# Performance work log

Measured on AMD Instinct MI355X. Metric: run time of the kernel, lower is better.

## Reference

```python
import jax, jax.numpy as jnp
import numpy as np

B, C4, H, W = 2, 128, 128, 128
POOL_SIZE = 10


def setup_inputs() -> dict:
    key = jax.random.key(0)
    k1, k2, k3 = jax.random.split(key, 3)
    feature = jax.random.normal(k1, (B, C4, H, W), dtype=jnp.float32)
    K = H * W
    # valid boxes: x1<x2, y1<y2, inside the feature map
    xy1 = jax.random.uniform(k2, (B, K, 2), dtype=jnp.float32) * jnp.array([W * 0.5, H * 0.5], jnp.float32)
    wh = jax.random.uniform(k3, (B, K, 2), dtype=jnp.float32) * jnp.array([W * 0.45, H * 0.45], jnp.float32) + 1.0
    boxes = jnp.concatenate([xy1, xy1 + wh], axis=-1)  # [B, K, 4] = (x1,y1,x2,y2)
    return {"feature": feature, "boxes": boxes, "pool_size": POOL_SIZE}


def reference(feature, boxes, pool_size):
    # feature: [B, 4*C, H, W]; boxes: [B, K, 4]; output: [B, C, K, 4]
    Bn, C4n, Hn, Wn = feature.shape
    C = C4n // 4
    K = boxes.shape[1]
    P = pool_size + 1
    x1, y1, x2, y2 = (boxes[..., i] for i in range(4))  # each [B, K]
    t = jnp.arange(P, dtype=feature.dtype) / pool_size  # [P]
    sx = x1[..., None] + t * (x2 - x1)[..., None]  # [B, K, P] along-x samples
    sy = y1[..., None] + t * (y2 - y1)[..., None]  # [B, K, P] along-y samples
    cx1 = jnp.broadcast_to(x1[..., None], sx.shape)
    cx2 = jnp.broadcast_to(x2[..., None], sx.shape)
    cy1 = jnp.broadcast_to(y1[..., None], sy.shape)
    cy2 = jnp.broadcast_to(y2[..., None], sy.shape)
    # border order: 0=top (y=y1), 1=left (x=x1), 2=bottom (y=y2), 3=right (x=x2)
    xs = jnp.stack([sx, cx1, sx, cx2], axis=1)  # [B, 4, K, P]
    ys = jnp.stack([cy1, sy, cy2, sy], axis=1)  # [B, 4, K, P]

    valid = (xs > -1.0) & (xs < Wn) & (ys > -1.0) & (ys < Hn)
    x = jnp.clip(xs, 0.0, Wn - 1)
    y = jnp.clip(ys, 0.0, Hn - 1)
    x0 = jnp.floor(x).astype(jnp.int32)
    y0 = jnp.floor(y).astype(jnp.int32)
    x1i = jnp.minimum(x0 + 1, Wn - 1)
    y1i = jnp.minimum(y0 + 1, Hn - 1)
    lx = (x - x0)[:, :, None]  # [B, 4, 1, K, P]
    ly = (y - y0)[:, :, None]

    featf = feature.reshape(Bn, 4, C, Hn * Wn)  # channel group g feeds border g

    def gather(yi, xi):
        idx = (yi * Wn + xi).reshape(Bn, 4, 1, K * P)
        return jnp.take_along_axis(featf, idx, axis=3).reshape(Bn, 4, C, K, P)

    val = (gather(y0, x0) * (1 - ly) * (1 - lx)
           + gather(y0, x1i) * (1 - ly) * lx
           + gather(y1i, x0) * ly * (1 - lx)
           + gather(y1i, x1i) * ly * lx)
    val = jnp.where(valid[:, :, None], val, 0.0)
    out = val.max(axis=-1)  # max-pool over the P samples per border -> [B, 4, C, K]
    return out.transpose(0, 2, 3, 1)  # [B, C, K, 4]
```

## Files before the change

kernel.cpp:

```cpp
#include <hip/hip_runtime.h>
#include <math.h>

#define BN   2
#define CG   32
#define HH   128
#define WW   128
#define HWSZ (HH*WW)
#define KK   16384
#define CHUNK 256
#define NCHK 2
#define SORTB 64
#define SEGCAP 32

#define WS_F16_OFF   (0u)
#define WS_TMP_OFF   (8u << 20)
#define WS_BKT_OFF   (16u << 20)
#define WS_CNT_OFF   (32u << 20)
#define WS_NEED      ((32u << 20) + (128u << 10))

typedef float vf4 __attribute__((ext_vector_type(4)));
typedef _Float16 h8 __attribute__((ext_vector_type(8)));

__device__ inline unsigned int pack_h2(float a, float b) {
  unsigned short ua = __builtin_bit_cast(unsigned short, (_Float16)a);
  unsigned short ub = __builtin_bit_cast(unsigned short, (_Float16)b);
  return (unsigned int)ua | ((unsigned int)ub << 16);
}

__global__ __launch_bounds__(256) void sort_transpose_kernel(
    const float* __restrict__ feat, unsigned short* __restrict__ ws,
    const float* __restrict__ boxes, unsigned int* __restrict__ cnt,
    uint4* __restrict__ bkt) {
  __shared__ uint2 smem[128 * 9];
  const int blk = blockIdx.x;
  const int t   = threadIdx.x;

  if (blk < SORTB) {
    unsigned int* hist = (unsigned int*)smem;
    const int batch = blk >> 5;
    const int seg   = blk & 31;
    const int k0    = seg * 512;
    hist[t] = 0u; hist[t + 256] = 0u;
    __syncthreads();

    vf4 bx[2];
    unsigned short rnk[2][4];
    int bin[2][4];
#pragma unroll
    for (int i = 0; i < 2; ++i) {
      const int k = k0 + i * 256 + t;
      bx[i] = *(const vf4*)(boxes + ((size_t)batch * KK + k) * 4);
#pragma unroll
      for (int g = 0; g < 4; ++g) {
        const float fix = (g == 0) ? bx[i][1] : (g == 1) ? bx[i][0]
                         : (g == 2) ? bx[i][3] : bx[i][2];
        const int f0 = (int)fminf(fmaxf(fix, 0.0f), 127.0f);
        bin[i][g] = (g << 7) | f0;
        rnk[i][g] = (unsigned short)atomicAdd(&hist[bin[i][g]], 1u);
      }
    }
    __syncthreads();

    cnt[(size_t)((batch << 9) + t) * 32 + seg]       = min(hist[t], (unsigned)SEGCAP);
    cnt[(size_t)((batch << 9) + t + 256) * 32 + seg] = min(hist[t + 256], (unsigned)SEGCAP);

#pragma unroll
    for (int i = 0; i < 2; ++i) {
      const int k = k0 + i * 256 + t;
#pragma unroll
      for (int g = 0; g < 4; ++g) {
        if (rnk[i][g] < SEGCAP) {
          const bool horiz = (g & 1) == 0;
          const float fix = (g == 0) ? bx[i][1] : (g == 1) ? bx[i][0]
                           : (g == 2) ? bx[i][3] : bx[i][2];
          const float fc = fminf(fmaxf(fix, 0.0f), 127.0f);
          const int f0 = bin[i][g] & 127;
          const float mov_s = horiz ? bx[i][0] : bx[i][1];
          const float mov_d = horiz ? (bx[i][2] - bx[i][0]) : (bx[i][3] - bx[i][1]);
          const float lf    = fc - (float)f0;
          const bool  fok   = (fix > -1.0f) && (fix < 128.0f);
          uint4 rec;
          rec.x = __builtin_bit_cast(unsigned int, mov_s);
          rec.y = __builtin_bit_cast(unsigned int, mov_d);
          rec.z = __builtin_bit_cast(unsigned int, lf);
          rec.w = (unsigned int)k | (fok ? 0x80000000u : 0u);
          const int gbin = (batch << 9) + bin[i][g];
          bkt[(size_t)gbin * (32 * SEGCAP) + seg * SEGCAP + rnk[i][g]] = rec;
        }
      }
    }
  } else {
    uint2* lds = smem;
    const int idx = blk - SORTB;
    const int s  = idx & 7;
    const int i0 = (idx >> 3) * 128;

    const int iL = (t & 31) * 4;
    const int cq = t >> 5;

    const float* src = feat + (size_t)s * (CG * HWSZ) + i0 + iL;
    vf4 r[4];
#pragma unroll
    for (int cc = 0; cc < 4; ++cc)
      r[cc] = *(const vf4*)(src + (size_t)(cq * 4 + cc) * HWSZ);

#pragma unroll
    for (int ii = 0; ii < 4; ++ii) {
      uint2 q;
      q.x = pack_h2(r[0][ii], r[1][ii]);
      q.y = pack_h2(r[2][ii], r[3][ii]);
      lds[(iL + ii) * 9 + cq] = q;
    }
    __syncthreads();

    uint2* dst = (uint2*)(ws + ((size_t)s * HWSZ + i0) * CG);
    const int q2 = t & 7;
    const int ih = t >> 3;
#pragma unroll
    for (int it = 0; it < 4; ++it) {
      const int i = ih + 32 * it;
      dst[i * 8 + q2] = lds[i * 9 + q2];
    }
  }
}

__global__ __launch_bounds__(256) void border_gather_binned(
    const unsigned short* __restrict__ wsu,
    const unsigned int* __restrict__ cnt, const uint4* __restrict__ bkt,
    const int* __restrict__ psp, unsigned short* __restrict__ tmp) {
  __shared__ _Float16 tile[2 * 128 * 40];
  __shared__ uint4 recs[CHUNK];
  __shared__ unsigned int segbase[33];
  __shared__ float stf[64];

  const int blk  = blockIdx.x;
  const int s    = blk & 7;
  const int f0   = (blk >> 3) & 127;
  const int ch   = blk >> 10;
  const int g    = s & 3;
  const int b    = s >> 2;
  const int gbin = s * 128 + f0;
  const int t    = threadIdx.x;

  if (t < 64) {
    unsigned int c = 0u;
    if (t < 32) c = min(cnt[(size_t)gbin * 32 + t], (unsigned)SEGCAP);
    unsigned int x = c;
#pragma unroll
    for (int d = 1; d < 32; d <<= 1) {
      unsigned int y = __shfl_up(x, d, 64);
      if (t >= d) x += y;
    }
    if (t < 32) {
      segbase[t] = x - c;
      if (t == 31) segbase[32] = x;
    }
  }
  __syncthreads();

  const int n  = (int)segbase[32];
  const int i0 = ch * CHUNK;
  const int i1 = min(n, i0 + CHUNK);
  if (i1 <= i0) return;

  const int ps = *psp;
  if (t < 64) stf[t] = (float)(t <= ps ? t : ps) / (float)ps;

  const bool horiz = (g & 1) == 0;
  const int f1 = min(f0 + 1, 127);
  const _Float16* slab = (const _Float16*)wsu + (size_t)s * (HWSZ * CG);

#pragma unroll
  for (int it = 0; it < 4; ++it) {
    const int chunk = it * 256 + t;
    const int cc   = chunk >> 9;
    const int rem  = chunk & 511;
    const int p    = rem >> 2;
    const int slot = rem & 3;
    const int fcc  = cc ? f1 : f0;
    const size_t srci = horiz ? ((size_t)(fcc * 128 + p) * 32)
                              : ((size_t)(p * 128 + fcc) * 32);
    const uint4 v = *(const uint4*)(slab + srci + slot * 8);
    *(uint4*)((char*)tile + cc * 10240 + p * 80 + slot * 16) = v;
  }

  {
    const int s2 = t >> 3;
    const int j  = t & 7;
    const int base = (int)segbase[s2];
    const int c    = (int)segbase[s2 + 1] - base;
    for (int l = j; l < c; l += 8) {
      const int pos = base + l;
      if (pos >= i0 && pos < i1)
        recs[pos - i0] = bkt[(size_t)gbin * (32 * SEGCAP) + s2 * SEGCAP + l];
    }
  }
  __syncthreads();

  const int w      = t >> 6;
  const int oct    = t & 3;
  const int slot16 = (t >> 2) & 15;

  for (int base = i0 + w * 16; base < i1; base += 64) {
    const int ii  = base + slot16;
    const bool vb = ii < i1;
    const uint4 rec = recs[vb ? (ii - i0) : 0];
    const float mov_s = __builtin_bit_cast(float, rec.x);
    const float mov_d = __builtin_bit_cast(float, rec.y);
    const float lf    = __builtin_bit_cast(float, rec.z);
    const bool  fok   = (rec.w >> 31) != 0u;
    const int   kid   = (int)(rec.w & 0xFFFFu);

    h8 acc = (h8)(_Float16)(-65504.0f);

#define SAMPLE(TP) do {                                                    \
      const float mov = fmaf((TP), mov_d, mov_s);                          \
      const bool ok = fok && (mov > -1.0f) && (mov < 128.0f);              \
      const float mc = fminf(fmaxf(mov, 0.0f), 127.0f);                    \
      const int m0 = (int)mc;                                              \
      const float lm = mc - (float)m0;                                     \
      const int m1 = min(m0 + 1, 127);                                     \
      const int a0 = m0 * 80 + oct * 16;                                   \
      const int a1 = m1 * 80 + oct * 16;                                   \
      const h8 f00 = *(const h8*)((const char*)tile + a0);                 \
      const h8 f01 = *(const h8*)((const char*)tile + a1);                 \
      const h8 f10 = *(const h8*)((const char*)tile + 10240 + a0);         \
      const h8 f11 = *(const h8*)((const char*)tile + 10240 + a1);         \
      const _Float16 w00 = (_Float16)((1.0f - lf) * (1.0f - lm));          \
      const _Float16 w01 = (_Float16)((1.0f - lf) * lm);                   \
      const _Float16 w10 = (_Float16)(lf * (1.0f - lm));                   \
      const _Float16 w11 = (_Float16)(lf * lm);                            \
      h8 v = f00 * w00 + f01 * w01 + f10 * w10 + f11 * w11;                \
      v = ok ? v : (h8)(_Float16)0.0f;                                     \
      acc = __builtin_elementwise_max(acc, v);                             \
    } while (0)

    if (ps == 10) {
#pragma unroll
      for (int p = 0; p <= 10; ++p) SAMPLE((float)p / 10.0f);
    } else {
      for (int p = 0; p <= ps; ++p) SAMPLE(stf[p]);
    }
#undef SAMPLE

    if (vb) {
      h8* dst = (h8*)(tmp + ((size_t)(b * 4 + g) * KK + kid) * 32 + oct * 8);
      *dst = acc;
    }
  }
}

__global__ __launch_bounds__(256) void untranspose_kernel(
    const unsigned short* __restrict__ tmp, float* __restrict__ out) {
  __shared__ float lds[4 * 32 * 33];
  const int blk = blockIdx.x;
  const int b   = blk >> 9;
  const int k0  = (blk & 511) * 32;
  const int t   = threadIdx.x;

#pragma unroll
  for (int it = 0; it < 2; ++it) {
    const int chunk = it * 256 + t;
    const int g   = chunk >> 7;
    const int rem = chunk & 127;
    const int kk  = rem >> 2;
    const int co8 = rem & 3;
    const h8 v = *(const h8*)((const _Float16*)tmp
                 + ((size_t)(b * 4 + g) * KK + k0 + kk) * 32 + co8 * 8);
#pragma unroll
    for (int j = 0; j < 8; ++j)
      lds[g * (32 * 33) + kk * 33 + co8 * 8 + j] = (float)v[j];
  }
  __syncthreads();

#pragma unroll
  for (int it = 0; it < 4; ++it) {
    const int chunk = it * 256 + t;
    const int c  = chunk >> 5;
    const int kk = chunk & 31;
    vf4 v;
#pragma unroll
    for (int g = 0; g < 4; ++g)
      v[g] = lds[g * (32 * 33) + kk * 33 + c];
    vf4* dst = (vf4*)(out + ((size_t)(b * CG + c) * KK + k0 + kk) * 4);
    __builtin_nontemporal_store(v, dst);
  }
}

__global__ __launch_bounds__(128) void border_align_fallback(
    const float* __restrict__ base, const float* __restrict__ boxes,
    const int* __restrict__ psp, float* __restrict__ out) {
  const int blk = blockIdx.x;
  const int b = blk >> 10;
  const int t = threadIdx.x;
  const int g = t >> 5, c = t & 31;
  const int k0 = (blk & 1023) * 16;
  const int ps = *psp;
  const float psf = (float)ps;
  const float* slab = base + (size_t)(b * 4 + g) * (CG * HWSZ) + (size_t)c * HWSZ;
  for (int kk = 0; kk < 16; ++kk) {
    const int kbox = k0 + kk;
    const float x1 = boxes[((size_t)b * KK + kbox) * 4 + 0];
    const float y1 = boxes[((size_t)b * KK + kbox) * 4 + 1];
    const float x2 = boxes[((size_t)b * KK + kbox) * 4 + 2];
    const float y2 = boxes[((size_t)b * KK + kbox) * 4 + 3];
    float m = -INFINITY;
    for (int p = 0; p <= ps; ++p) {
      const float tf = (float)p / psf;
      float x, y;
      if      (g == 0) { x = x1 + tf * (x2 - x1); y = y1; }
      else if (g == 1) { x = x1; y = y1 + tf * (y2 - y1); }
      else if (g == 2) { x = x1 + tf * (x2 - x1); y = y2; }
      else             { x = x2; y = y1 + tf * (y2 - y1); }
      const bool valid = (x > -1.0f) && (x < 128.0f) && (y > -1.0f) && (y < 128.0f);
      const float xc = fminf(fmaxf(x, 0.0f), 127.0f);
      const float yc = fminf(fmaxf(y, 0.0f), 127.0f);
      const int x0 = (int)xc, y0 = (int)yc;
      const float lx = xc - (float)x0, ly = yc - (float)y0;
      const int x1i = min(x0 + 1, 127), y1i = min(y0 + 1, 127);
      const float f00 = slab[y0 * WW + x0],  f01 = slab[y0 * WW + x1i];
      const float f10 = slab[y1i * WW + x0], f11 = slab[y1i * WW + x1i];
      float v = f00 * (1 - ly) * (1 - lx) + f01 * (1 - ly) * lx
              + f10 * ly * (1 - lx) + f11 * ly * lx;
      v = valid ? v : 0.0f;
      m = fmaxf(m, v);
    }
    out[(((size_t)(b * CG + c)) * KK + kbox) * 4 + g] = m;
  }
}

extern "C" void kernel_launch(void* const* d_in, const int* in_sizes, int n_in,
                              void* d_out, int out_size, void* d_ws, size_t ws_size,
                              hipStream_t stream) {
  const float* feature = (const float*)d_in[0];
  const float* boxes   = (const float*)d_in[1];
  const int*   psp     = (const int*)d_in[2];
  float*       out     = (float*)d_out;

  if (ws_size >= WS_NEED) {
    char* ws = (char*)d_ws;
    unsigned short* wsf16 = (unsigned short*)(ws + WS_F16_OFF);
    unsigned short* tmp   = (unsigned short*)(ws + WS_TMP_OFF);
    uint4*          bkt   = (uint4*)(ws + WS_BKT_OFF);
    unsigned int*   cnt   = (unsigned int*)(ws + WS_CNT_OFF);

    hipLaunchKernelGGL(sort_transpose_kernel, dim3(SORTB + 8 * (HWSZ / 128)),
                       dim3(256), 0, stream, feature, wsf16, boxes, cnt, bkt);
    hipLaunchKernelGGL(border_gather_binned, dim3(NCHK * 1024), dim3(256), 0,
                       stream, wsf16, cnt, bkt, psp, tmp);
    hipLaunchKernelGGL(untranspose_kernel, dim3(BN * 512), dim3(256), 0, stream,
                       tmp, out);
  } else {
    hipLaunchKernelGGL(border_align_fallback, dim3(BN * (KK / 16)), dim3(128), 0,
                       stream, feature, boxes, psp, out);
  }
}
```

Before: 91.52 us.

## Fuse three stages into one cooperative persistent kernel with grid syncs

New measurement: 336.3 us. 3.67x slower.

```diff
diff --git a/kernel.cpp b/kernel.cpp
--- a/kernel.cpp
+++ b/kernel.cpp
@@ -1,5 +1,8 @@
 #include <hip/hip_runtime.h>
+#include <hip/hip_cooperative_groups.h>
 #include <math.h>
+
+namespace cg = cooperative_groups;
 
 #define BN   2
 #define CG   32
@@ -11,6 +14,7 @@
 #define NCHK 2
 #define SORTB 64
 #define SEGCAP 32
+#define GRID 1024
 
 #define WS_F16_OFF   (0u)
 #define WS_TMP_OFF   (8u << 20)
@@ -18,6 +22,12 @@
 #define WS_CNT_OFF   (32u << 20)
 #define WS_NEED      ((32u << 20) + (128u << 10))
 
+#define SM_TILE   0
+#define SM_RECS   20480
+#define SM_SEGB   24576
+#define SM_STF    24712
+#define SM_SIZE   25088
+
 typedef float vf4 __attribute__((ext_vector_type(4)));
 typedef _Float16 h8 __attribute__((ext_vector_type(8)));
 
@@ -27,120 +37,115 @@
   return (unsigned int)ua | ((unsigned int)ub << 16);
 }
 
-__global__ __launch_bounds__(256) void sort_transpose_kernel(
-    const float* __restrict__ feat, unsigned short* __restrict__ ws,
-    const float* __restrict__ boxes, unsigned int* __restrict__ cnt,
-    uint4* __restrict__ bkt) {
-  __shared__ uint2 smem[128 * 9];
-  const int blk = blockIdx.x;
-  const int t   = threadIdx.x;
-
-  if (blk < SORTB) {
-    unsigned int* hist = (unsigned int*)smem;
-    const int batch = blk >> 5;
-    const int seg   = blk & 31;
-    const int k0    = seg * 512;
-    hist[t] = 0u; hist[t + 256] = 0u;
-    __syncthreads();
-
-    vf4 bx[2];
-    unsigned short rnk[2][4];
-    int bin[2][4];
-#pragma unroll
-    for (int i = 0; i < 2; ++i) {
-      const int k = k0 + i * 256 + t;
-      bx[i] = *(const vf4*)(boxes + ((size_t)batch * KK + k) * 4);
-#pragma unroll
-      for (int g = 0; g < 4; ++g) {
+
+__device__ __forceinline__ void sort_body(
+    char* smem, int v, const float* __restrict__ boxes,
+    unsigned int* __restrict__ cnt, uint4* __restrict__ bkt, int t) {
+  unsigned int* hist = (unsigned int*)smem;
+  const int batch = v >> 5;
+  const int seg   = v & 31;
+  const int k0    = seg * 512;
+  hist[t] = 0u; hist[t + 256] = 0u;
+  __syncthreads();
+
+  vf4 bx[2];
+  unsigned short rnk[2][4];
+  int bin[2][4];
+#pragma unroll
+  for (int i = 0; i < 2; ++i) {
+    const int k = k0 + i * 256 + t;
+    bx[i] = *(const vf4*)(boxes + ((size_t)batch * KK + k) * 4);
+#pragma unroll
+    for (int g = 0; g < 4; ++g) {
+      const float fix = (g == 0) ? bx[i][1] : (g == 1) ? bx[i][0]
+                       : (g == 2) ? bx[i][3] : bx[i][2];
+      const int f0 = (int)fminf(fmaxf(fix, 0.0f), 127.0f);
+      bin[i][g] = (g << 7) | f0;
+      rnk[i][g] = (unsigned short)atomicAdd(&hist[bin[i][g]], 1u);
+    }
+  }
+  __syncthreads();
+
+  cnt[(size_t)((batch << 9) + t) * 32 + seg]       = min(hist[t], (unsigned)SEGCAP);
+  cnt[(size_t)((batch << 9) + t + 256) * 32 + seg] = min(hist[t + 256], (unsigned)SEGCAP);
+
+#pragma unroll
+  for (int i = 0; i < 2; ++i) {
+    const int k = k0 + i * 256 + t;
+#pragma unroll
+    for (int g = 0; g < 4; ++g) {
+      if (rnk[i][g] < SEGCAP) {
+        const bool horiz = (g & 1) == 0;
         const float fix = (g == 0) ? bx[i][1] : (g == 1) ? bx[i][0]
                          : (g == 2) ? bx[i][3] : bx[i][2];
-        const int f0 = (int)fminf(fmaxf(fix, 0.0f), 127.0f);
-        bin[i][g] = (g << 7) | f0;
-        rnk[i][g] = (unsigned short)atomicAdd(&hist[bin[i][g]], 1u);
+        const float fc = fminf(fmaxf(fix, 0.0f), 127.0f);
+        const int f0 = bin[i][g] & 127;
+        const float mov_s = horiz ? bx[i][0] : bx[i][1];
+        const float mov_d = horiz ? (bx[i][2] - bx[i][0]) : (bx[i][3] - bx[i][1]);
+        const float lf    = fc - (float)f0;
+        const bool  fok   = (fix > -1.0f) && (fix < 128.0f);
+        uint4 rec;
+        rec.x = __builtin_bit_cast(unsigned int, mov_s);
+        rec.y = __builtin_bit_cast(unsigned int, mov_d);
+        rec.z = __builtin_bit_cast(unsigned int, lf);
+        rec.w = (unsigned int)k | (fok ? 0x80000000u : 0u);
+        const int gbin = (batch << 9) + bin[i][g];
+        bkt[(size_t)gbin * (32 * SEGCAP) + seg * SEGCAP + rnk[i][g]] = rec;
       }
     }
-    __syncthreads();
-
-    cnt[(size_t)((batch << 9) + t) * 32 + seg]       = min(hist[t], (unsigned)SEGCAP);
-    cnt[(size_t)((batch << 9) + t + 256) * 32 + seg] = min(hist[t + 256], (unsigned)SEGCAP);
-
-#pragma unroll
-    for (int i = 0; i < 2; ++i) {
-      const int k = k0 + i * 256 + t;
-#pragma unroll
-      for (int g = 0; g < 4; ++g) {
-        if (rnk[i][g] < SEGCAP) {
-          const bool horiz = (g & 1) == 0;
-          const float fix = (g == 0) ? bx[i][1] : (g == 1) ? bx[i][0]
-                           : (g == 2) ? bx[i][3] : bx[i][2];
-          const float fc = fminf(fmaxf(fix, 0.0f), 127.0f);
-          const int f0 = bin[i][g] & 127;
-          const float mov_s = horiz ? bx[i][0] : bx[i][1];
-          const float mov_d = horiz ? (bx[i][2] - bx[i][0]) : (bx[i][3] - bx[i][1]);
-          const float lf    = fc - (float)f0;
-          const bool  fok   = (fix > -1.0f) && (fix < 128.0f);
-          uint4 rec;
-          rec.x = __builtin_bit_cast(unsigned int, mov_s);
-          rec.y = __builtin_bit_cast(unsigned int, mov_d);
-          rec.z = __builtin_bit_cast(unsigned int, lf);
-          rec.w = (unsigned int)k | (fok ? 0x80000000u : 0u);
-          const int gbin = (batch << 9) + bin[i][g];
-          bkt[(size_t)gbin * (32 * SEGCAP) + seg * SEGCAP + rnk[i][g]] = rec;
-        }
-      }
-    }
-  } else {
-    uint2* lds = smem;
-    const int idx = blk - SORTB;
-    const int s  = idx & 7;
-    const int i0 = (idx >> 3) * 128;
-
-    const int iL = (t & 31) * 4;
-    const int cq = t >> 5;
-
-    const float* src = feat + (size_t)s * (CG * HWSZ) + i0 + iL;
-    vf4 r[4];
-#pragma unroll
-    for (int cc = 0; cc < 4; ++cc)
-      r[cc] = *(const vf4*)(src + (size_t)(cq * 4 + cc) * HWSZ);
-
-#pragma unroll
-    for (int ii = 0; ii < 4; ++ii) {
-      uint2 q;
-      q.x = pack_h2(r[0][ii], r[1][ii]);
-      q.y = pack_h2(r[2][ii], r[3][ii]);
-      lds[(iL + ii) * 9 + cq] = q;
-    }
-    __syncthreads();
-
-    uint2* dst = (uint2*)(ws + ((size_t)s * HWSZ + i0) * CG);
-    const int q2 = t & 7;
-    const int ih = t >> 3;
-#pragma unroll
-    for (int it = 0; it < 4; ++it) {
-      const int i = ih + 32 * it;
-      dst[i * 8 + q2] = lds[i * 9 + q2];
-    }
-  }
-}
-
-__global__ __launch_bounds__(256) void border_gather_binned(
-    const unsigned short* __restrict__ wsu,
+  }
+}
+
+__device__ __forceinline__ void transpose_body(
+    char* smem, int idx, const float* __restrict__ feat,
+    unsigned short* __restrict__ ws, int t) {
+  uint2* lds = (uint2*)smem;
+  const int s  = idx & 7;
+  const int i0 = (idx >> 3) * 128;
+
+  const int iL = (t & 31) * 4;
+  const int cq = t >> 5;
+
+  const float* src = feat + (size_t)s * (CG * HWSZ) + i0 + iL;
+  vf4 r[4];
+#pragma unroll
+  for (int cc = 0; cc < 4; ++cc)
+    r[cc] = *(const vf4*)(src + (size_t)(cq * 4 + cc) * HWSZ);
+
+#pragma unroll
+  for (int ii = 0; ii < 4; ++ii) {
+    uint2 q;
+    q.x = pack_h2(r[0][ii], r[1][ii]);
+    q.y = pack_h2(r[2][ii], r[3][ii]);
+    lds[(iL + ii) * 9 + cq] = q;
+  }
+  __syncthreads();
+
+  uint2* dst = (uint2*)(ws + ((size_t)s * HWSZ + i0) * CG);
+  const int q2 = t & 7;
+  const int ih = t >> 3;
+#pragma unroll
+  for (int it = 0; it < 4; ++it) {
+    const int i = ih + 32 * it;
+    dst[i * 8 + q2] = lds[i * 9 + q2];
+  }
+}
+
+__device__ __forceinline__ void gather_body(
+    char* smem, int v, const unsigned short* __restrict__ wsu,
     const unsigned int* __restrict__ cnt, const uint4* __restrict__ bkt,
-    const int* __restrict__ psp, unsigned short* __restrict__ tmp) {
-  __shared__ _Float16 tile[2 * 128 * 40];
-  __shared__ uint4 recs[CHUNK];
-  __shared__ unsigned int segbase[33];
-  __shared__ float stf[64];
-
-  const int blk  = blockIdx.x;
-  const int s    = blk & 7;
-  const int f0   = (blk >> 3) & 127;
-  const int ch   = blk >> 10;
+    const int* __restrict__ psp, unsigned short* __restrict__ tmp, int t) {
+  _Float16* tile = (_Float16*)(smem + SM_TILE);
+  uint4* recs    = (uint4*)(smem + SM_RECS);
+  unsigned int* segbase = (unsigned int*)(smem + SM_SEGB);
+  float* stf     = (float*)(smem + SM_STF);
+
+  const int s    = v & 7;
+  const int f0   = (v >> 3) & 127;
+  const int ch   = v >> 10;
   const int g    = s & 3;
   const int b    = s >> 2;
   const int gbin = s * 128 + f0;
-  const int t    = threadIdx.x;
 
   if (t < 64) {
     unsigned int c = 0u;
@@ -180,8 +185,8 @@
     const int fcc  = cc ? f1 : f0;
     const size_t srci = horiz ? ((size_t)(fcc * 128 + p) * 32)
                               : ((size_t)(p * 128 + fcc) * 32);
-    const uint4 v = *(const uint4*)(slab + srci + slot * 8);
-    *(uint4*)((char*)tile + cc * 10240 + p * 80 + slot * 16) = v;
+    const uint4 vq = *(const uint4*)(slab + srci + slot * 8);
+    *(uint4*)((char*)tile + cc * 10240 + p * 80 + slot * 16) = vq;
   }
 
   {
@@ -230,9 +235,9 @@
       const _Float16 w01 = (_Float16)((1.0f - lf) * lm);                   \
       const _Float16 w10 = (_Float16)(lf * (1.0f - lm));                   \
       const _Float16 w11 = (_Float16)(lf * lm);                            \
-      h8 v = f00 * w00 + f01 * w01 + f10 * w10 + f11 * w11;                \
-      v = ok ? v : (h8)(_Float16)0.0f;                                     \
-      acc = __builtin_elementwise_max(acc, v);                             \
+      h8 vv = f00 * w00 + f01 * w01 + f10 * w10 + f11 * w11;               \
+      vv = ok ? vv : (h8)(_Float16)0.0f;                                   \
+      acc = __builtin_elementwise_max(acc, vv);                            \
     } while (0)
 
     if (ps == 10) {
@@ -250,13 +255,12 @@
   }
 }
 
-__global__ __launch_bounds__(256) void untranspose_kernel(
-    const unsigned short* __restrict__ tmp, float* __restrict__ out) {
-  __shared__ float lds[4 * 32 * 33];
-  const int blk = blockIdx.x;
-  const int b   = blk >> 9;
-  const int k0  = (blk & 511) * 32;
-  const int t   = threadIdx.x;
+__device__ __forceinline__ void untranspose_body(
+    char* smem, int v, const unsigned short* __restrict__ tmp,
+    float* __restrict__ out, int t) {
+  float* lds = (float*)smem;
+  const int b   = v >> 9;
+  const int k0  = (v & 511) * 32;
 
 #pragma unroll
   for (int it = 0; it < 2; ++it) {
@@ -265,11 +269,11 @@
     const int rem = chunk & 127;
     const int kk  = rem >> 2;
     const int co8 = rem & 3;
-    const h8 v = *(const h8*)((const _Float16*)tmp
+    const h8 vv = *(const h8*)((const _Float16*)tmp
                  + ((size_t)(b * 4 + g) * KK + k0 + kk) * 32 + co8 * 8);
 #pragma unroll
     for (int j = 0; j < 8; ++j)
-      lds[g * (32 * 33) + kk * 33 + co8 * 8 + j] = (float)v[j];
+      lds[g * (32 * 33) + kk * 33 + co8 * 8 + j] = (float)vv[j];
   }
   __syncthreads();
 
@@ -278,13 +282,64 @@
     const int chunk = it * 256 + t;
     const int c  = chunk >> 5;
     const int kk = chunk & 31;
-    vf4 v;
+    vf4 vv;
 #pragma unroll
     for (int g = 0; g < 4; ++g)
-      v[g] = lds[g * (32 * 33) + kk * 33 + c];
+      vv[g] = lds[g * (32 * 33) + kk * 33 + c];
     vf4* dst = (vf4*)(out + ((size_t)(b * CG + c) * KK + k0 + kk) * 4);
-    __builtin_nontemporal_store(v, dst);
-  }
+    __builtin_nontemporal_store(vv, dst);
+  }
+}
+
+__global__ __launch_bounds__(256, 4) void fused_border_align(
+    const float* __restrict__ feat, unsigned short* __restrict__ ws,
+    const float* __restrict__ boxes, unsigned int* __restrict__ cnt,
+    uint4* __restrict__ bkt, const int* __restrict__ psp,
+    unsigned short* __restrict__ tmp, float* __restrict__ out) {
+  cg::grid_group grid = cg::this_grid();
+  __shared__ __align__(16) char smem[SM_SIZE];
+  const int t = threadIdx.x;
+
+  for (int v = blockIdx.x; v < SORTB + 1024; v += GRID) {
+    __syncthreads();
+    if (v < SORTB) sort_body(smem, v, boxes, cnt, bkt, t);
+    else           transpose_body(smem, v - SORTB, feat, ws, t);
+  }
+  grid.sync();
+
+  for (int v = blockIdx.x; v < NCHK * 1024; v += GRID) {
+    __syncthreads();
+    gather_body(smem, v, ws, cnt, bkt, psp, tmp, t);
+  }
+  grid.sync();
+
+  __syncthreads();
+  untranspose_body(smem, blockIdx.x, tmp, out, t);
+}
+
+__global__ __launch_bounds__(256) void sort_transpose_kernel(
+    const float* __restrict__ feat, unsigned short* __restrict__ ws,
+    const float* __restrict__ boxes, unsigned int* __restrict__ cnt,
+    uint4* __restrict__ bkt) {
+  __shared__ __align__(16) char smem[9216];
+  const int blk = blockIdx.x;
+  const int t   = threadIdx.x;
+  if (blk < SORTB) sort_body(smem, blk, boxes, cnt, bkt, t);
+  else             transpose_body(smem, blk - SORTB, feat, ws, t);
+}
+
+__global__ __launch_bounds__(256) void border_gather_binned(
+    const unsigned short* __restrict__ wsu,
+    const unsigned int* __restrict__ cnt, const uint4* __restrict__ bkt,
+    const int* __restrict__ psp, unsigned short* __restrict__ tmp) {
+  __shared__ __align__(16) char smem[SM_SIZE];
+  gather_body(smem, blockIdx.x, wsu, cnt, bkt, psp, tmp, threadIdx.x);
+}
+
+__global__ __launch_bounds__(256) void untranspose_kernel(
+    const unsigned short* __restrict__ tmp, float* __restrict__ out) {
+  __shared__ __align__(16) char smem[16896];
+  untranspose_body(smem, blockIdx.x, tmp, out, threadIdx.x);
 }
 
 __global__ __launch_bounds__(128) void border_align_fallback(
@@ -344,12 +399,20 @@
     uint4*          bkt   = (uint4*)(ws + WS_BKT_OFF);
     unsigned int*   cnt   = (unsigned int*)(ws + WS_CNT_OFF);
 
-    hipLaunchKernelGGL(sort_transpose_kernel, dim3(SORTB + 8 * (HWSZ / 128)),
-                       dim3(256), 0, stream, feature, wsf16, boxes, cnt, bkt);
-    hipLaunchKernelGGL(border_gather_binned, dim3(NCHK * 1024), dim3(256), 0,
-                       stream, wsf16, cnt, bkt, psp, tmp);
-    hipLaunchKernelGGL(untranspose_kernel, dim3(BN * 512), dim3(256), 0, stream,
-                       tmp, out);
+    void* args[] = {(void*)&feature, (void*)&wsf16, (void*)&boxes,
+                    (void*)&cnt, (void*)&bkt, (void*)&psp,
+                    (void*)&tmp, (void*)&out};
+    hipError_t err = hipLaunchCooperativeKernel(
+        (const void*)fused_border_align, dim3(GRID), dim3(256), args, 0,
+        stream);
+    if (err != hipSuccess) {
+      hipLaunchKernelGGL(sort_transpose_kernel, dim3(SORTB + 8 * (HWSZ / 128)),
+                         dim3(256), 0, stream, feature, wsf16, boxes, cnt, bkt);
+      hipLaunchKernelGGL(border_gather_binned, dim3(NCHK * 1024), dim3(256), 0,
+                         stream, wsf16, cnt, bkt, psp, tmp);
+      hipLaunchKernelGGL(untranspose_kernel, dim3(BN * 512), dim3(256), 0,
+                         stream, tmp, out);
+    }
   } else {
     hipLaunchKernelGGL(border_align_fallback, dim3(BN * (KK / 16)), dim3(128), 0,
                        stream, feature, boxes, psp, out);
```
